# Performance work log

Hardware: AMD Instinct MI355X
Metric: run time of the kernel (lower is better)

Reference implementation:

```python
import jax, jax.numpy as jnp
import numpy as np

N = 100000
E = 640000
D = 128

def setup_inputs() -> dict:
    key = jax.random.key(0)
    ks = jax.random.split(key, 12)
    s = 1.0 / np.sqrt(D)
    inp = {
        'x': jax.random.normal(ks[0], (N, D), dtype=jnp.float32),
        'edge_index': jax.random.randint(ks[1], (2, E), 0, N, dtype=jnp.int64),
    }
    names = ['W1l', 'b1', 'W1r', 'W2l', 'b2', 'W2r', 'W3l', 'b3', 'W3r']
    shapes = [(D, D), (D,), (D, D), (D, D), (D,), (D, D), (D, D), (D,), (D, D)]
    for i, (n, sh) in enumerate(zip(names, shapes)):
        inp[n] = jax.random.normal(ks[2 + i], sh, dtype=jnp.float32) * s
    return inp

def _sage_conv(x, src, dst, Wl, b, Wr):
    # mean aggregation of source features at destination nodes
    msg = x[src]                                            # [E, D] gather
    agg = jax.ops.segment_sum(msg, dst, num_segments=N)     # [N, D]
    cnt = jax.ops.segment_sum(jnp.ones((src.shape[0],), x.dtype), dst, num_segments=N)
    agg = agg / jnp.maximum(cnt, 1.0)[:, None]
    # lin_l(aggr) + lin_r(x); bias lives in lin_l (PyG default)
    return agg @ Wl.T + b + x @ Wr.T

def reference(x, edge_index, W1l, b1, W1r, W2l, b2, W2r, W3l, b3, W3r):
    src, dst = edge_index[0], edge_index[1]
    h = jax.nn.relu(_sage_conv(x, src, dst, W1l, b1, W1r))
    # dropout layers are identity in eval mode
    h = jax.nn.relu(_sage_conv(h, src, dst, W2l, b2, W2r))
    h = _sage_conv(h, src, dst, W3l, b3, W3r)
    return h
```

## Files before the change

### kernel.cpp

```cpp
#include <hip/hip_runtime.h>


typedef __attribute__((ext_vector_type(8))) short bf16x8;
typedef __attribute__((ext_vector_type(4))) float f32x4;
typedef __attribute__((ext_vector_type(4))) unsigned int u32x4;

__device__ __forceinline__ unsigned short f2bf(float f) {
  unsigned u = __float_as_uint(f);
  u += 0x7fffu + ((u >> 16) & 1u);
  return (unsigned short)(u >> 16);
}

__global__ __launch_bounds__(256) void cvt_kernel(const float* __restrict__ in,
                                                  unsigned short* __restrict__ out, int n8) {
  int i = blockIdx.x * 256 + threadIdx.x;
  if (i >= n8) return;
  const float4* p = (const float4*)(in + (size_t)i * 8);
  float4 a = p[0], b = p[1];
  union { unsigned short s[8]; u32x4 u; } pk;
  pk.s[0] = f2bf(a.x); pk.s[1] = f2bf(a.y); pk.s[2] = f2bf(a.z); pk.s[3] = f2bf(a.w);
  pk.s[4] = f2bf(b.x); pk.s[5] = f2bf(b.y); pk.s[6] = f2bf(b.z); pk.s[7] = f2bf(b.w);
  *(u32x4*)(out + (size_t)i * 8) = pk.u;
}

__global__ __launch_bounds__(256) void count_kernel(const int* __restrict__ dst,
                                                    int* __restrict__ cnt, int E) {
  int e = blockIdx.x * 256 + threadIdx.x;
  if (e < E) atomicAdd(&cnt[dst[e]], 1);
}

__global__ __launch_bounds__(256) void partial_kernel(const int* __restrict__ cnt,
                                                      int* __restrict__ blocksum, int N) {
  __shared__ int red[256];
  int t = threadIdx.x;
  int idx = blockIdx.x * 2048 + t * 8;
  int s = 0;
  if (idx + 8 <= N) {
    int4 a = *(const int4*)(cnt + idx);
    int4 b = *(const int4*)(cnt + idx + 4);
    s = a.x + a.y + a.z + a.w + b.x + b.y + b.z + b.w;
  } else {
    for (int i = idx; i < N && i < idx + 8; ++i) s += cnt[i];
  }
  red[t] = s;
  __syncthreads();
  for (int off = 128; off > 0; off >>= 1) {
    if (t < off) red[t] += red[t + off];
    __syncthreads();
  }
  if (t == 0) blocksum[blockIdx.x] = red[0];
}

__global__ __launch_bounds__(64) void scanmid_kernel(const int* __restrict__ blocksum,
                                                     int* __restrict__ blockoff, int nb) {
  int l = threadIdx.x;
  int own = (l < nb) ? blocksum[l] : 0;
  int v = own;
  for (int off = 1; off < 64; off <<= 1) {
    int u = __shfl_up(v, off);
    if (l >= off) v += u;
  }
  if (l < nb) blockoff[l] = v - own;
}

__global__ __launch_bounds__(256) void final_kernel(const int* __restrict__ cnt,
                                                    const int* __restrict__ blockoff,
                                                    int* __restrict__ rowstart,
                                                    int* __restrict__ cursor,
                                                    float* __restrict__ inv, int N) {
  __shared__ int thr[256];
  int t = threadIdx.x;
  int idx = blockIdx.x * 2048 + t * 8;
  int c[8];
  int s = 0;
#pragma unroll
  for (int i = 0; i < 8; ++i) {
    int n = idx + i;
    c[i] = (n < N) ? cnt[n] : 0;
    s += c[i];
  }
  thr[t] = s;
  __syncthreads();
  for (int off = 1; off < 256; off <<= 1) {
    int u = (t >= off) ? thr[t - off] : 0;
    __syncthreads();
    thr[t] += u;
    __syncthreads();
  }
  int run = blockoff[blockIdx.x] + thr[t] - s;
#pragma unroll
  for (int i = 0; i < 8; ++i) {
    int n = idx + i;
    if (n < N) {
      rowstart[n] = run;
      cursor[n] = run;
      inv[n] = 1.f / fmaxf((float)c[i], 1.f);
      run += c[i];
      if (n == N - 1) rowstart[N] = run;
    }
  }
}

__global__ __launch_bounds__(256) void fill_kernel(const int* __restrict__ src,
                                                   const int* __restrict__ dst,
                                                   int* __restrict__ cursor,
                                                   int* __restrict__ elist, int E) {
  int e = blockIdx.x * 256 + threadIdx.x;
  if (e < E) {
    int d = dst[e];
    int pos = atomicAdd(&cursor[d], 1);
    elist[pos] = src[e];
  }
}

__global__ __launch_bounds__(256) void aggregate_kernel(const unsigned short* __restrict__ xbf,
                                                        const int* __restrict__ rowstart,
                                                        const int* __restrict__ elist,
                                                        const float* __restrict__ inv,
                                                        unsigned short* __restrict__ aggbf, int N) {
  int gid = blockIdx.x * 256 + threadIdx.x;
  int node = gid >> 6;
  if (node >= N) return;
  int lane = threadIdx.x & 63;
  int grp = lane >> 4;
  int l16 = lane & 15;

  int beg = rowstart[node], end = rowstart[node + 1];
  float acc[8];
#pragma unroll
  for (int j = 0; j < 8; ++j) acc[j] = 0.f;

  for (int e = beg + grp; e < end; e += 4) {
    int s = elist[e];
    u32x4 u = *(const u32x4*)(xbf + ((size_t)s << 7) + l16 * 8);
#pragma unroll
    for (int d = 0; d < 4; ++d) {
      acc[2 * d]     += __uint_as_float(u[d] << 16);
      acc[2 * d + 1] += __uint_as_float(u[d] & 0xffff0000u);
    }
  }

#pragma unroll
  for (int j = 0; j < 8; ++j) {
    acc[j] += __shfl_xor(acc[j], 16);
    acc[j] += __shfl_xor(acc[j], 32);
  }

  if (grp == 0) {
    float iv = inv[node];
    union { unsigned short s[8]; u32x4 u; } pk;
#pragma unroll
    for (int j = 0; j < 8; ++j) pk.s[j] = f2bf(acc[j] * iv);
    *(u32x4*)(aggbf + ((size_t)node << 7) + l16 * 8) = pk.u;
  }
}

__global__ __launch_bounds__(256, 2) void sage_gemm(
    const unsigned short* __restrict__ Abf, const unsigned short* __restrict__ Xbf,
    const float* __restrict__ Wl, const float* __restrict__ Wr, const float* __restrict__ bias,
    float* __restrict__ outf, unsigned short* __restrict__ outb, int N, int relu) {
  __shared__ __align__(16) unsigned short sW[2][128][128];
  const int tid = threadIdx.x;
  for (int it = tid; it < 4096; it += 256) {
    int m = it >> 11;
    int o = (it >> 4) & 127;
    int ch = it & 15;
    const float* wsrc = (m ? Wr : Wl) + o * 128 + ch * 8;
    float4 f0 = *(const float4*)wsrc;
    float4 f1 = *(const float4*)(wsrc + 4);
    union { unsigned short s[8]; u32x4 u; } pk;
    pk.s[0] = f2bf(f0.x); pk.s[1] = f2bf(f0.y); pk.s[2] = f2bf(f0.z); pk.s[3] = f2bf(f0.w);
    pk.s[4] = f2bf(f1.x); pk.s[5] = f2bf(f1.y); pk.s[6] = f2bf(f1.z); pk.s[7] = f2bf(f1.w);
    *(u32x4*)&sW[m][o][(ch ^ (o & 15)) << 3] = pk.u;
  }
  __syncthreads();

  const int l = tid & 63;
  const int w = tid >> 6;
  const int l15 = l & 15;
  const int lg = l >> 4;
  const int row_base = blockIdx.x * 256 + w * 64;

  f32x4 acc[4][8];
#pragma unroll
  for (int rt = 0; rt < 4; ++rt)
#pragma unroll
    for (int ot = 0; ot < 8; ++ot) acc[rt][ot] = f32x4{0.f, 0.f, 0.f, 0.f};

  union frag { u32x4 u; bf16x8 v; };

  int rrow[4];
#pragma unroll
  for (int rt = 0; rt < 4; ++rt) {
    int r = row_base + rt * 16 + l15;
    rrow[rt] = (r < N) ? r : (N - 1);
  }

#pragma unroll
  for (int h = 0; h < 2; ++h) {
    const unsigned short* Asrc = h ? Xbf : Abf;
#pragma unroll
    for (int ks = 0; ks < 4; ++ks) {
      frag af[4];
#pragma unroll
      for (int rt = 0; rt < 4; ++rt)
        af[rt].u = *(const u32x4*)(Asrc + ((size_t)rrow[rt] << 7) + (ks * 32 + lg * 8));
      frag bq[8];
#pragma unroll
      for (int ot = 0; ot < 8; ++ot)
        bq[ot].u = *(const u32x4*)&sW[h][ot * 16 + l15][((((ks << 2) | lg) ^ l15)) << 3];
#pragma unroll
      for (int rt = 0; rt < 4; ++rt)
#pragma unroll
        for (int ot = 0; ot < 8; ++ot)
          acc[rt][ot] = __builtin_amdgcn_mfma_f32_16x16x32_bf16(af[rt].v, bq[ot].v, acc[rt][ot], 0, 0, 0);
    }
  }

  float bv[8];
#pragma unroll
  for (int ot = 0; ot < 8; ++ot) bv[ot] = bias[ot * 16 + l15];

#pragma unroll
  for (int rt = 0; rt < 4; ++rt) {
#pragma unroll
    for (int i = 0; i < 4; ++i) {
      int r = row_base + rt * 16 + lg * 4 + i;
      if (r < N) {
#pragma unroll
        for (int ot = 0; ot < 8; ++ot) {
          float v = acc[rt][ot][i] + bv[ot];
          if (relu) v = fmaxf(v, 0.f);
          size_t idx = ((size_t)r << 7) + ot * 16 + l15;
          if (outf) outf[idx] = v;
          else outb[idx] = f2bf(v);
        }
      }
    }
  }
}

extern "C" void kernel_launch(void* const* d_in, const int* in_sizes, int n_in,
                              void* d_out, int out_size, void* d_ws, size_t ws_size,
                              hipStream_t stream) {
  (void)n_in; (void)out_size; (void)ws_size;
  const float* x = (const float*)d_in[0];
  const int* ei = (const int*)d_in[1];
  const float* W1l = (const float*)d_in[2];
  const float* b1 = (const float*)d_in[3];
  const float* W1r = (const float*)d_in[4];
  const float* W2l = (const float*)d_in[5];
  const float* b2 = (const float*)d_in[6];
  const float* W2r = (const float*)d_in[7];
  const float* W3l = (const float*)d_in[8];
  const float* b3 = (const float*)d_in[9];
  const float* W3r = (const float*)d_in[10];
  float* out = (float*)d_out;

  const int N = in_sizes[0] / 128;
  const int E = in_sizes[1] / 2;
  const int* srcp = ei;
  const int* dstp = ei + E;

  char* ws = (char*)d_ws;
  size_t off = 0;
  auto alloc = [&](size_t bytes) {
    void* p = ws + off;
    off = (off + bytes + 255) & ~(size_t)255;
    return p;
  };
  unsigned short* bufA = (unsigned short*)alloc((size_t)N * 128 * 2);
  unsigned short* bufB = (unsigned short*)alloc((size_t)N * 128 * 2);
  unsigned short* aggbf = (unsigned short*)alloc((size_t)N * 128 * 2);
  int* cnt = (int*)alloc((size_t)N * 4);
  int* rowstart = (int*)alloc((size_t)(N + 1) * 4);
  int* cursor = (int*)alloc((size_t)N * 4);
  float* inv = (float*)alloc((size_t)N * 4);
  int* elist = (int*)alloc((size_t)E * 4);
  int* blocksum = (int*)alloc(64 * 4);
  int* blockoff = (int*)alloc(64 * 4);

  const int nb = (N + 2047) / 2048;

  hipMemsetAsync(cnt, 0, (size_t)N * 4, stream);
  cvt_kernel<<<(N * 128 / 8 + 255) / 256, 256, 0, stream>>>(x, bufA, N * 128 / 8);
  count_kernel<<<(E + 255) / 256, 256, 0, stream>>>(dstp, cnt, E);
  partial_kernel<<<nb, 256, 0, stream>>>(cnt, blocksum, N);
  scanmid_kernel<<<1, 64, 0, stream>>>(blocksum, blockoff, nb);
  final_kernel<<<nb, 256, 0, stream>>>(cnt, blockoff, rowstart, cursor, inv, N);
  fill_kernel<<<(E + 255) / 256, 256, 0, stream>>>(srcp, dstp, cursor, elist, E);

  int aggBlocks = (N + 3) / 4;
  int gemmBlocks = (N + 255) / 256;

  aggregate_kernel<<<aggBlocks, 256, 0, stream>>>(bufA, rowstart, elist, inv, aggbf, N);
  sage_gemm<<<gemmBlocks, 256, 0, stream>>>(aggbf, bufA, W1l, W1r, b1, nullptr, bufB, N, 1);
  aggregate_kernel<<<aggBlocks, 256, 0, stream>>>(bufB, rowstart, elist, inv, aggbf, N);
  sage_gemm<<<gemmBlocks, 256, 0, stream>>>(aggbf, bufB, W2l, W2r, b2, nullptr, bufA, N, 1);
  aggregate_kernel<<<aggBlocks, 256, 0, stream>>>(bufA, rowstart, elist, inv, aggbf, N);
  sage_gemm<<<gemmBlocks, 256, 0, stream>>>(aggbf, bufA, W3l, W3r, b3, out, nullptr, N, 0);
}
```

Before: 396.6 us.

## Partition CSR atomics by destination range and use 16 lanes per node in aggregation

The count and fill kernels now launch a fixed grid of 1024 blocks. Blocks are split into 8 partitions by blockIdx low bits, and each partition performs atomics only for destinations in its slice of the node range. The goal is to localise atomic traffic per XCD/L2 and reduce cross-die contention. The aggregation kernel now assigns one 16-lane group per node instead of a 64-lane wavefront with four edge groups and a shuffle reduction, unrolling two edges per iteration. This removes shuffles and idle lanes but gives less memory-level parallelism per node, and every partition now reads the full edge list.

```diff
diff --git a/kernel.cpp b/kernel.cpp
--- a/kernel.cpp
+++ b/kernel.cpp
@@ -24,9 +24,16 @@
 }
 
 __global__ __launch_bounds__(256) void count_kernel(const int* __restrict__ dst,
-                                                    int* __restrict__ cnt, int E) {
-  int e = blockIdx.x * 256 + threadIdx.x;
-  if (e < E) atomicAdd(&cnt[dst[e]], 1);
+                                                    int* __restrict__ cnt, int E, float pscale) {
+  int p = blockIdx.x & 7;
+  int blk = blockIdx.x >> 3;
+  int stride = (gridDim.x >> 3) * 256;
+  for (int e = blk * 256 + threadIdx.x; e < E; e += stride) {
+    int d = dst[e];
+    int pd = (int)((float)d * pscale);
+    pd = pd > 7 ? 7 : pd;
+    if (pd == p) atomicAdd(&cnt[d], 1);
+  }
 }
 
 __global__ __launch_bounds__(256) void partial_kernel(const int* __restrict__ cnt,
@@ -104,12 +111,19 @@
 __global__ __launch_bounds__(256) void fill_kernel(const int* __restrict__ src,
                                                    const int* __restrict__ dst,
                                                    int* __restrict__ cursor,
-                                                   int* __restrict__ elist, int E) {
-  int e = blockIdx.x * 256 + threadIdx.x;
-  if (e < E) {
+                                                   int* __restrict__ elist, int E, float pscale) {
+  int p = blockIdx.x & 7;
+  int blk = blockIdx.x >> 3;
+  int stride = (gridDim.x >> 3) * 256;
+  for (int e = blk * 256 + threadIdx.x; e < E; e += stride) {
     int d = dst[e];
-    int pos = atomicAdd(&cursor[d], 1);
-    elist[pos] = src[e];
+    int s = src[e];
+    int pd = (int)((float)d * pscale);
+    pd = pd > 7 ? 7 : pd;
+    if (pd == p) {
+      int pos = atomicAdd(&cursor[d], 1);
+      elist[pos] = s;
+    }
   }
 }
 
@@ -119,40 +133,44 @@
                                                         const float* __restrict__ inv,
                                                         unsigned short* __restrict__ aggbf, int N) {
   int gid = blockIdx.x * 256 + threadIdx.x;
-  int node = gid >> 6;
+  int node = gid >> 4;
   if (node >= N) return;
-  int lane = threadIdx.x & 63;
-  int grp = lane >> 4;
-  int l16 = lane & 15;
+  int l16 = threadIdx.x & 15;
 
   int beg = rowstart[node], end = rowstart[node + 1];
   float acc[8];
 #pragma unroll
   for (int j = 0; j < 8; ++j) acc[j] = 0.f;
 
-  for (int e = beg + grp; e < end; e += 4) {
-    int s = elist[e];
-    u32x4 u = *(const u32x4*)(xbf + ((size_t)s << 7) + l16 * 8);
+  int e = beg;
+  for (; e + 2 <= end; e += 2) {
+    int s0 = elist[e];
+    int s1 = elist[e + 1];
+    u32x4 u0 = *(const u32x4*)(xbf + ((size_t)s0 << 7) + l16 * 8);
+    u32x4 u1 = *(const u32x4*)(xbf + ((size_t)s1 << 7) + l16 * 8);
 #pragma unroll
     for (int d = 0; d < 4; ++d) {
-      acc[2 * d]     += __uint_as_float(u[d] << 16);
-      acc[2 * d + 1] += __uint_as_float(u[d] & 0xffff0000u);
-    }
-  }
-
-#pragma unroll
-  for (int j = 0; j < 8; ++j) {
-    acc[j] += __shfl_xor(acc[j], 16);
-    acc[j] += __shfl_xor(acc[j], 32);
-  }
-
-  if (grp == 0) {
-    float iv = inv[node];
-    union { unsigned short s[8]; u32x4 u; } pk;
-#pragma unroll
-    for (int j = 0; j < 8; ++j) pk.s[j] = f2bf(acc[j] * iv);
-    *(u32x4*)(aggbf + ((size_t)node << 7) + l16 * 8) = pk.u;
-  }
+      acc[2 * d]     += __uint_as_float(u0[d] << 16);
+      acc[2 * d + 1] += __uint_as_float(u0[d] & 0xffff0000u);
+      acc[2 * d]     += __uint_as_float(u1[d] << 16);
+      acc[2 * d + 1] += __uint_as_float(u1[d] & 0xffff0000u);
+    }
+  }
+  if (e < end) {
+    int s0 = elist[e];
+    u32x4 u0 = *(const u32x4*)(xbf + ((size_t)s0 << 7) + l16 * 8);
+#pragma unroll
+    for (int d = 0; d < 4; ++d) {
+      acc[2 * d]     += __uint_as_float(u0[d] << 16);
+      acc[2 * d + 1] += __uint_as_float(u0[d] & 0xffff0000u);
+    }
+  }
+
+  float iv = inv[node];
+  union { unsigned short s[8]; u32x4 u; } pk;
+#pragma unroll
+  for (int j = 0; j < 8; ++j) pk.s[j] = f2bf(acc[j] * iv);
+  *(u32x4*)(aggbf + ((size_t)node << 7) + l16 * 8) = pk.u;
 }
 
 __global__ __launch_bounds__(256, 2) void sage_gemm(
@@ -261,6 +279,7 @@
   const int E = in_sizes[1] / 2;
   const int* srcp = ei;
   const int* dstp = ei + E;
+  const float pscale = 8.0f / (float)N;
 
   char* ws = (char*)d_ws;
   size_t off = 0;
@@ -284,13 +303,13 @@
 
   hipMemsetAsync(cnt, 0, (size_t)N * 4, stream);
   cvt_kernel<<<(N * 128 / 8 + 255) / 256, 256, 0, stream>>>(x, bufA, N * 128 / 8);
-  count_kernel<<<(E + 255) / 256, 256, 0, stream>>>(dstp, cnt, E);
+  count_kernel<<<1024, 256, 0, stream>>>(dstp, cnt, E, pscale);
   partial_kernel<<<nb, 256, 0, stream>>>(cnt, blocksum, N);
   scanmid_kernel<<<1, 64, 0, stream>>>(blocksum, blockoff, nb);
   final_kernel<<<nb, 256, 0, stream>>>(cnt, blockoff, rowstart, cursor, inv, N);
-  fill_kernel<<<(E + 255) / 256, 256, 0, stream>>>(srcp, dstp, cursor, elist, E);
-
-  int aggBlocks = (N + 3) / 4;
+  fill_kernel<<<1024, 256, 0, stream>>>(srcp, dstp, cursor, elist, E, pscale);
+
+  int aggBlocks = (N * 16 + 255) / 256;
   int gemmBlocks = (N + 255) / 256;
 
   aggregate_kernel<<<aggBlocks, 256, 0, stream>>>(bufA, rowstart, elist, inv, aggbf, N);
```

After: 358.4 us. 9.6% less time.
